# Kernel tuning notes

Measured on AMD Instinct MI355X. Metric: run time of the kernel, lower is better.

Reference implementation:

```python
import math
import jax, jax.numpy as jnp
import numpy as np

B, L, S, H, E, D = 2, 2048, 2048, 16, 64, 64

def setup_inputs() -> dict:
    key = jax.random.key(0)
    k1, k2, k3, k4, k5 = jax.random.split(key, 5)
    return {
        "queries": jax.random.normal(k1, (B, L, H, E), dtype=jnp.float32),
        "keys": jax.random.normal(k2, (B, S, H, E), dtype=jnp.float32),
        "values": jax.random.normal(k3, (B, S, H, D), dtype=jnp.float32),
        "tau": jax.random.uniform(k4, (B, 1), dtype=jnp.float32),
        "delta": jax.random.normal(k5, (B, S), dtype=jnp.float32),
        "attn_mask": jnp.zeros((1,), dtype=jnp.bool_),
    }

def reference(queries, keys, values, tau, delta, attn_mask):
    # queries: [B,L,H,E], keys: [B,S,H,E], values: [B,S,H,D]
    # tau: [B,1] -> [B,1,1,1]; delta: [B,S] -> [B,1,1,S]
    # mask_flag=False, so attn_mask is unused. Dropout is identity at eval.
    E_ = queries.shape[-1]
    scale = 1.0 / math.sqrt(E_)
    scores = jnp.einsum('blhe,bshe->bhls', queries, keys)  # [B,H,L,S]
    scores = scores * tau[:, None, None, :]                # de-stationary scale
    scores = scores + delta[:, None, None, :]              # de-stationary shift
    A = jax.nn.softmax(scale * scores, axis=-1)            # [B,H,L,S]
    V = jnp.einsum('bhls,bshd->blhd', A, values)           # [B,L,H,D]
    return V
```

## Files before the change

kernel.cpp:

```cpp
#include <hip/hip_runtime.h>


#define Bb 2
#define Ll 2048
#define Ss 2048
#define Hh 16
#define Ee 64
#define Dd 64
#define KV 64

typedef _Float16 f16x8 __attribute__((ext_vector_type(8)));
typedef _Float16 f16x4 __attribute__((ext_vector_type(4)));
typedef __fp16 fp16x2 __attribute__((ext_vector_type(2)));
typedef float f32x4 __attribute__((ext_vector_type(4)));

union Pk2 { fp16x2 h; unsigned u; };
union PackU { unsigned u[4]; f16x8 v; };

#define GLDS(gp, lp) __builtin_amdgcn_global_load_lds( \
    (const __attribute__((address_space(1))) void*)(gp), \
    (__attribute__((address_space(3))) void*)(lp), 16, 0, 0)

__global__ __launch_bounds__(256)
void prepass_k(const float* __restrict__ K, _Float16* __restrict__ K16,
               const float* __restrict__ delta, float* __restrict__ delta2)
{
    const unsigned v = blockIdx.x * 256 + threadIdx.x;
    const unsigned e4 = v & 15;
    const unsigned h  = (v >> 4) & 15;
    const unsigned s  = (v >> 8) & (Ss - 1);
    const unsigned b  = v >> 19;
    const f32x4 src = ((const f32x4*)K)[v];
    f16x4 t;
    t[0] = (_Float16)src[0]; t[1] = (_Float16)src[1];
    t[2] = (_Float16)src[2]; t[3] = (_Float16)src[3];
    ((f16x4*)K16)[(((size_t)(b * Hh + h) * Ss + s) * 16) + e4] = t;
    if (v < (Bb * Ss) / 4) {
        f32x4 dd = ((const f32x4*)delta)[v];
        ((f32x4*)delta2)[v] = (f32x4){0.125f * dd[0], 0.125f * dd[1],
                                      0.125f * dd[2], 0.125f * dd[3]};
    }
}

__global__ __launch_bounds__(256)
void prepass_v(const float* __restrict__ V, _Float16* __restrict__ VT16)
{
    __shared__ _Float16 TL[64][66];
    const int tid  = threadIdx.x;
    const int wave = tid >> 6;
    const int lane = tid & 63;
    const int bh = blockIdx.y;
    const int b  = bh >> 4;
    const int h  = bh & 15;
    const int s0 = blockIdx.x * 64;

    #pragma unroll
    for (int rr = 0; rr < 16; ++rr) {
        const int row = wave * 16 + rr;
        TL[row][lane] = (_Float16)V[((size_t)(b * Ss + s0 + row) * Hh + h) * Dd + lane];
    }
    __syncthreads();
    const int d  = tid >> 2;
    const int sq = (tid & 3) * 16;
    union { _Float16 h[16]; f16x8 v[2]; } tmp;
    #pragma unroll
    for (int i = 0; i < 16; ++i) tmp.h[i] = TL[sq + i][d];
    f16x8* dp = (f16x8*)(VT16 + ((size_t)(b * Hh + h) * Dd + d) * Ss + s0 + sq);
    dp[0] = tmp.v[0];
    dp[1] = tmp.v[1];
}

__global__ __launch_bounds__(256)
void dsattn_fwd_v3(const float* __restrict__ Q, const _Float16* __restrict__ K16,
                   const _Float16* __restrict__ VT16, const float* __restrict__ tau,
                   const float* __restrict__ delta2, float* __restrict__ out)
{
    extern __shared__ __align__(16) unsigned char smem[];

    const int tid  = threadIdx.x;
    const int wave = tid >> 6;
    const int lane = tid & 63;
    const int lq   = lane & 15;
    const int g    = lane >> 4;

    const int bh = blockIdx.y;
    const int b  = bh >> 4;
    const int h  = bh & 15;
    const int q0 = blockIdx.x * 64;

    const float alpha = 0.125f * tau[b];

    f16x8 aq[2];
    {
        const float* qp = Q + (((size_t)b * Ll + q0 + wave * 16 + lq) * Hh + h) * Ee;
        #pragma unroll
        for (int es = 0; es < 2; ++es) {
            const float* p = qp + es * 32 + g * 8;
            f16x8 t;
            #pragma unroll
            for (int j = 0; j < 8; ++j) t[j] = (_Float16)p[j];
            aq[es] = t;
        }
    }

    f32x4 osum[4];
    #pragma unroll
    for (int i = 0; i < 4; ++i) osum[i] = (f32x4){0.f, 0.f, 0.f, 0.f};
    float m_run = -1e30f, l_run = 0.0f;

    const unsigned char* kb  = (const unsigned char*)(K16 + (size_t)(b * Hh + h) * Ss * Ee);
    const unsigned char* vtb = (const unsigned char*)(VT16 + (size_t)(b * Hh + h) * Dd * Ss);
    const float* d2b = delta2 + (size_t)b * Ss;

    const int row0  = tid >> 3;
    const int slotS = (tid & 7) ^ (row0 & 7);

    {
        unsigned char* kw = smem + wave * 1024;
        unsigned char* vw = smem + 8192 + wave * 1024;
        GLDS(kb + (size_t)row0 * 128 + slotS * 16,        kw);
        GLDS(kb + (size_t)(row0 + 32) * 128 + slotS * 16, kw + 4096);
        GLDS(vtb + (size_t)row0 * (Ss * 2) + slotS * 16,        vw);
        GLDS(vtb + (size_t)(row0 + 32) * (Ss * 2) + slotS * 16, vw + 4096);
    }
    f32x4 dcur[4], dnxt[4];
    #pragma unroll
    for (int t = 0; t < 4; ++t)
        dcur[t] = *(const f32x4*)(d2b + t * 16 + 4 * g);
    __syncthreads();

    int cur = 0;
    for (int sb = 0; sb < Ss; sb += KV) {
        const int nb = (sb + KV < Ss);
        if (nb) {
            unsigned char* kw = smem + (cur ^ 1) * 16384 + wave * 1024;
            unsigned char* vw = kw + 8192;
            const int sn = sb + KV;
            GLDS(kb + (size_t)(sn + row0) * 128 + slotS * 16,        kw);
            GLDS(kb + (size_t)(sn + row0 + 32) * 128 + slotS * 16,   kw + 4096);
            GLDS(vtb + (size_t)row0 * (Ss * 2) + sn * 2 + slotS * 16,        vw);
            GLDS(vtb + (size_t)(row0 + 32) * (Ss * 2) + sn * 2 + slotS * 16, vw + 4096);
        }
        {
            const int sn = nb ? sb + KV : sb;
            #pragma unroll
            for (int t = 0; t < 4; ++t)
                dnxt[t] = *(const f32x4*)(d2b + sn + t * 16 + 4 * g);
        }

        const unsigned char* Ksm = smem + cur * 16384;
        const unsigned char* Vsm = Ksm + 8192;

        float p[16];
        float tmax = -1e30f;
        __builtin_amdgcn_s_setprio(1);
        f32x4 c4[4];
        #pragma unroll
        for (int t = 0; t < 4; ++t) {
            f32x4 c = (f32x4){0.f, 0.f, 0.f, 0.f};
            const int srow = t * 16 + lq;
            #pragma unroll
            for (int es = 0; es < 2; ++es) {
                const int slot = (es * 4 + g) ^ (srow & 7);
                f16x8 ak = *(const f16x8*)(Ksm + srow * 128 + slot * 16);
                c = __builtin_amdgcn_mfma_f32_16x16x32_f16(ak, aq[es], c, 0, 0, 0);
            }
            c4[t] = c;
        }
        __builtin_amdgcn_s_setprio(0);
        #pragma unroll
        for (int t = 0; t < 4; ++t)
            #pragma unroll
            for (int j = 0; j < 4; ++j) {
                float z = fmaf(alpha, c4[t][j], dcur[t][j]);
                p[t * 4 + j] = z;
                tmax = fmaxf(tmax, z);
            }

        tmax = fmaxf(tmax, __shfl_xor(tmax, 16));
        tmax = fmaxf(tmax, __shfl_xor(tmax, 32));
        if (!__all(tmax <= m_run + 8.0f)) {
            const float m_new = fmaxf(m_run, tmax);
            const float corr  = __expf(m_run - m_new);
            l_run *= corr;
            #pragma unroll
            for (int dt = 0; dt < 4; ++dt)
                #pragma unroll
                for (int j = 0; j < 4; ++j)
                    osum[dt][j] *= corr;
            m_run = m_new;
        }
        float psum = 0.f;
        #pragma unroll
        for (int i = 0; i < 16; ++i) { p[i] = __expf(p[i] - m_run); psum += p[i]; }
        psum += __shfl_xor(psum, 16);
        psum += __shfl_xor(psum, 32);
        l_run += psum;

        unsigned pk[8];
        #pragma unroll
        for (int t = 0; t < 4; ++t) {
            Pk2 u0, u1;
            u0.h = __builtin_amdgcn_cvt_pkrtz(p[4 * t], p[4 * t + 1]);
            u1.h = __builtin_amdgcn_cvt_pkrtz(p[4 * t + 2], p[4 * t + 3]);
            pk[t * 2] = u0.u;
            pk[t * 2 + 1] = u1.u;
        }
        const int srcA = lq + 32 * (g & 1);
        const int srcB = srcA + 16;
        const bool gh = (g >> 1);
        PackU bp[2];
        #pragma unroll
        for (int ks = 0; ks < 2; ++ks) {
            unsigned a0 = __shfl(pk[ks * 4 + 0], srcA), a1 = __shfl(pk[ks * 4 + 1], srcA);
            unsigned a2 = __shfl(pk[ks * 4 + 2], srcA), a3 = __shfl(pk[ks * 4 + 3], srcA);
            unsigned b0 = __shfl(pk[ks * 4 + 0], srcB), b1 = __shfl(pk[ks * 4 + 1], srcB);
            unsigned b2 = __shfl(pk[ks * 4 + 2], srcB), b3 = __shfl(pk[ks * 4 + 3], srcB);
            bp[ks].u[0] = gh ? a2 : a0;
            bp[ks].u[1] = gh ? a3 : a1;
            bp[ks].u[2] = gh ? b2 : b0;
            bp[ks].u[3] = gh ? b3 : b1;
        }

        __builtin_amdgcn_s_setprio(1);
        #pragma unroll
        for (int ks = 0; ks < 2; ++ks)
            #pragma unroll
            for (int dt = 0; dt < 4; ++dt) {
                const int vrow = dt * 16 + lq;
                const int slot = (ks * 4 + g) ^ (vrow & 7);
                f16x8 av = *(const f16x8*)(Vsm + vrow * 128 + slot * 16);
                osum[dt] = __builtin_amdgcn_mfma_f32_16x16x32_f16(av, bp[ks].v, osum[dt], 0, 0, 0);
            }
        __builtin_amdgcn_s_setprio(0);

        __syncthreads();
        cur ^= 1;
        #pragma unroll
        for (int t = 0; t < 4; ++t) dcur[t] = dnxt[t];
    }

    float (*Osm)[16][68] = (float (*)[16][68])smem;
    const float inv = 1.0f / l_run;
    #pragma unroll
    for (int dt = 0; dt < 4; ++dt)
        #pragma unroll
        for (int j = 0; j < 4; ++j)
            Osm[wave][lq][dt * 16 + 4 * g + j] = osum[dt][j] * inv;
    __syncthreads();
    {
        float* ob = out + (((size_t)b * Ll + q0 + wave * 16) * Hh + h) * Dd;
        #pragma unroll
        for (int r = 0; r < 16; ++r)
            ob[(size_t)r * (Hh * Dd) + lane] = Osm[wave][r][lane];
    }
}

__global__ __launch_bounds__(256)
void dsattn_fwd(const float* __restrict__ Q, const float* __restrict__ K,
                const float* __restrict__ V, const float* __restrict__ tau,
                const float* __restrict__ delta, float* __restrict__ out)
{
    __shared__ __align__(16) unsigned char Ksm[32 * 128];
    __shared__ __align__(16) unsigned char VTsm[64 * 80];
    __shared__ float dsm[32];
    __shared__ float Osm[4][16][68];

    const int tid  = threadIdx.x;
    const int wave = tid >> 6;
    const int lane = tid & 63;
    const int lq   = lane & 15;
    const int g    = lane >> 4;

    const int bh = blockIdx.y;
    const int b  = bh >> 4;
    const int h  = bh & 15;
    const int q0 = blockIdx.x * 64;

    const float alpha = 0.125f * tau[b];

    f16x8 aq[2];
    {
        const float* qp = Q + (((long)b * Ll + q0 + wave * 16 + lq) * Hh + h) * Ee;
        #pragma unroll
        for (int es = 0; es < 2; ++es) {
            const float* p = qp + es * 32 + g * 8;
            f16x8 t;
            #pragma unroll
            for (int j = 0; j < 8; ++j) t[j] = (_Float16)p[j];
            aq[es] = t;
        }
    }

    f32x4 osum[4];
    #pragma unroll
    for (int i = 0; i < 4; ++i) osum[i] = (f32x4){0.f, 0.f, 0.f, 0.f};
    float m_run = -1e30f, l_run = 0.0f;

    const float* kb = K + ((long)b * Ss * Hh + h) * Ee;
    const float* vb = V + ((long)b * Ss * Hh + h) * Dd;
    const float* db = delta + (long)b * Ss;

    const int kr    = tid >> 3;
    const int kc    = (tid & 7) * 8;
    const int kslot = (((tid & 7) ^ (kr & 7)) * 16);
    const int vd    = tid & 63;
    const int vsh   = tid >> 6;

    for (int sb = 0; sb < Ss; sb += 32) {
        __syncthreads();
        {
            const float* src = kb + (long)(sb + kr) * (Hh * Ee) + kc;
            f16x8 t;
            #pragma unroll
            for (int j = 0; j < 8; ++j) t[j] = (_Float16)src[j];
            *(f16x8*)(Ksm + kr * 128 + kslot) = t;
        }
        {
            const float* src = vb + (long)(sb + vsh * 8) * (Hh * Dd) + vd;
            f16x8 t;
            #pragma unroll
            for (int j = 0; j < 8; ++j) t[j] = (_Float16)src[j * (Hh * Dd)];
            *(f16x8*)(VTsm + vd * 80 + vsh * 16) = t;
        }
        if (tid < 32) dsm[tid] = 0.125f * db[sb + tid];
        __syncthreads();

        float p[8];
        float tmax = -1e30f;
        #pragma unroll
        for (int t = 0; t < 2; ++t) {
            f32x4 c = (f32x4){0.f, 0.f, 0.f, 0.f};
            #pragma unroll
            for (int es = 0; es < 2; ++es) {
                const int srow = t * 16 + lq;
                const int slot = ((es * 4 + g) ^ (srow & 7)) * 16;
                f16x8 ak = *(const f16x8*)(Ksm + srow * 128 + slot);
                c = __builtin_amdgcn_mfma_f32_16x16x32_f16(ak, aq[es], c, 0, 0, 0);
            }
            #pragma unroll
            for (int j = 0; j < 4; ++j) {
                float z = alpha * c[j] + dsm[t * 16 + 4 * g + j];
                p[t * 4 + j] = z;
                tmax = fmaxf(tmax, z);
            }
        }
        tmax = fmaxf(tmax, __shfl_xor(tmax, 16));
        tmax = fmaxf(tmax, __shfl_xor(tmax, 32));
        const float m_new = fmaxf(m_run, tmax);
        const float corr  = __expf(m_run - m_new);
        float psum = 0.f;
        #pragma unroll
        for (int i = 0; i < 8; ++i) { p[i] = __expf(p[i] - m_new); psum += p[i]; }
        psum += __shfl_xor(psum, 16);
        psum += __shfl_xor(psum, 32);
        l_run = l_run * corr + psum;
        m_run = m_new;
        #pragma unroll
        for (int dt = 0; dt < 4; ++dt)
            #pragma unroll
            for (int j = 0; j < 4; ++j)
                osum[dt][j] *= corr;

        Pk2 u00, u01, u10, u11;
        u00.h = __builtin_amdgcn_cvt_pkrtz(p[0], p[1]);
        u01.h = __builtin_amdgcn_cvt_pkrtz(p[2], p[3]);
        u10.h = __builtin_amdgcn_cvt_pkrtz(p[4], p[5]);
        u11.h = __builtin_amdgcn_cvt_pkrtz(p[6], p[7]);
        const int srcA = lq + 32 * (g & 1);
        const int srcB = srcA + 16;
        unsigned a00 = __shfl(u00.u, srcA), a01 = __shfl(u01.u, srcA);
        unsigned a10 = __shfl(u10.u, srcA), a11 = __shfl(u11.u, srcA);
        unsigned b00 = __shfl(u00.u, srcB), b01 = __shfl(u01.u, srcB);
        unsigned b10 = __shfl(u10.u, srcB), b11 = __shfl(u11.u, srcB);
        const bool hi = (g >= 2);
        PackU bp;
        bp.u[0] = hi ? a10 : a00;
        bp.u[1] = hi ? a11 : a01;
        bp.u[2] = hi ? b10 : b00;
        bp.u[3] = hi ? b11 : b01;

        #pragma unroll
        for (int dt = 0; dt < 4; ++dt) {
            f16x8 av = *(const f16x8*)(VTsm + (dt * 16 + lq) * 80 + g * 16);
            osum[dt] = __builtin_amdgcn_mfma_f32_16x16x32_f16(av, bp.v, osum[dt], 0, 0, 0);
        }
    }

    const float inv = 1.0f / l_run;
    #pragma unroll
    for (int dt = 0; dt < 4; ++dt)
        #pragma unroll
        for (int j = 0; j < 4; ++j)
            Osm[wave][lq][dt * 16 + 4 * g + j] = osum[dt][j] * inv;
    __syncthreads();
    {
        float* ob = out + (((long)b * Ll + q0 + wave * 16) * Hh + h) * Dd;
        #pragma unroll
        for (int r = 0; r < 16; ++r)
            ob[(long)r * (Hh * Dd) + lane] = Osm[wave][r][lane];
    }
}

extern "C" void kernel_launch(void* const* d_in, const int* in_sizes, int n_in,
                              void* d_out, int out_size, void* d_ws, size_t ws_size,
                              hipStream_t stream) {
    const float* Q     = (const float*)d_in[0];
    const float* K     = (const float*)d_in[1];
    const float* V     = (const float*)d_in[2];
    const float* tau   = (const float*)d_in[3];
    const float* delta = (const float*)d_in[4];
    float* out = (float*)d_out;

    const size_t elems = (size_t)Bb * Hh * Ss * Ee;
    const size_t need  = elems * 2 * 2 + (size_t)Bb * Ss * 4;
    dim3 grid(Ll / 64, Bb * Hh);

    if (ws_size >= need) {
        _Float16* K16    = (_Float16*)d_ws;
        _Float16* VT16   = K16 + elems;
        float*    delta2 = (float*)(VT16 + elems);
        hipLaunchKernelGGL(prepass_k, dim3(elems / 4 / 256), dim3(256), 0, stream,
                           K, K16, delta, delta2);
        hipLaunchKernelGGL(prepass_v, dim3(Ss / 64, Bb * Hh), dim3(256), 0, stream, V, VT16);
        hipLaunchKernelGGL(dsattn_fwd_v3, grid, dim3(256), 32768, stream,
                           Q, K16, VT16, tau, delta2, out);
    } else {
        hipLaunchKernelGGL(dsattn_fwd, grid, dim3(256), 0, stream, Q, K, V, tau, delta, out);
    }
}
```

Baseline: 95.96 us.

## Process two query groups per wave to reuse K/V tiles across MFMAs

Each wave now handles 32 query rows as two 16-row groups, so the block tile grows to 128 queries. Every K and V fragment loaded from LDS now feeds two MFMAs, and each query row gets its own online-softmax state. This aims to halve the K/V global and LDS traffic per query and to give the scheduler more independent MFMA work. The trade-off is higher register pressure and half as many blocks in the grid.

```diff
diff --git a/kernel.cpp b/kernel.cpp
--- a/kernel.cpp
+++ b/kernel.cpp
@@ -71,7 +71,7 @@
 }
 
 __global__ __launch_bounds__(256)
-void dsattn_fwd_v3(const float* __restrict__ Q, const _Float16* __restrict__ K16,
+void dsattn_fwd_v4(const float* __restrict__ Q, const _Float16* __restrict__ K16,
                    const _Float16* __restrict__ VT16, const float* __restrict__ tau,
                    const float* __restrict__ delta2, float* __restrict__ out)
 {
@@ -86,27 +86,32 @@
     const int bh = blockIdx.y;
     const int b  = bh >> 4;
     const int h  = bh & 15;
-    const int q0 = blockIdx.x * 64;
+    const int q0 = blockIdx.x * 128;
+    const int qw = q0 + wave * 32;
 
     const float alpha = 0.125f * tau[b];
 
-    f16x8 aq[2];
-    {
-        const float* qp = Q + (((size_t)b * Ll + q0 + wave * 16 + lq) * Hh + h) * Ee;
+    f16x8 aq[2][2];
+    #pragma unroll
+    for (int qg = 0; qg < 2; ++qg) {
+        const float* qp = Q + (((size_t)b * Ll + qw + qg * 16 + lq) * Hh + h) * Ee;
         #pragma unroll
         for (int es = 0; es < 2; ++es) {
             const float* p = qp + es * 32 + g * 8;
             f16x8 t;
             #pragma unroll
             for (int j = 0; j < 8; ++j) t[j] = (_Float16)p[j];
-            aq[es] = t;
-        }
-    }
-
-    f32x4 osum[4];
-    #pragma unroll
-    for (int i = 0; i < 4; ++i) osum[i] = (f32x4){0.f, 0.f, 0.f, 0.f};
-    float m_run = -1e30f, l_run = 0.0f;
+            aq[qg][es] = t;
+        }
+    }
+
+    f32x4 osum[2][4];
+    #pragma unroll
+    for (int qg = 0; qg < 2; ++qg)
+        #pragma unroll
+        for (int i = 0; i < 4; ++i) osum[qg][i] = (f32x4){0.f, 0.f, 0.f, 0.f};
+    float m_run[2] = {-1e30f, -1e30f};
+    float l_run[2] = {0.0f, 0.0f};
 
     const unsigned char* kb  = (const unsigned char*)(K16 + (size_t)(b * Hh + h) * Ss * Ee);
     const unsigned char* vtb = (const unsigned char*)(VT16 + (size_t)(b * Hh + h) * Dd * Ss);
@@ -128,6 +133,10 @@
     for (int t = 0; t < 4; ++t)
         dcur[t] = *(const f32x4*)(d2b + t * 16 + 4 * g);
     __syncthreads();
+
+    const int srcA = lq + 32 * (g & 1);
+    const int srcB = srcA + 16;
+    const bool gh = (g >> 1);
 
     int cur = 0;
     for (int sb = 0; sb < Ss; sb += KV) {
@@ -151,75 +160,78 @@
         const unsigned char* Ksm = smem + cur * 16384;
         const unsigned char* Vsm = Ksm + 8192;
 
-        float p[16];
-        float tmax = -1e30f;
+        f32x4 c4[2][4];
+        #pragma unroll
+        for (int qg = 0; qg < 2; ++qg)
+            #pragma unroll
+            for (int t = 0; t < 4; ++t) c4[qg][t] = (f32x4){0.f, 0.f, 0.f, 0.f};
         __builtin_amdgcn_s_setprio(1);
-        f32x4 c4[4];
         #pragma unroll
         for (int t = 0; t < 4; ++t) {
-            f32x4 c = (f32x4){0.f, 0.f, 0.f, 0.f};
             const int srow = t * 16 + lq;
             #pragma unroll
             for (int es = 0; es < 2; ++es) {
                 const int slot = (es * 4 + g) ^ (srow & 7);
                 f16x8 ak = *(const f16x8*)(Ksm + srow * 128 + slot * 16);
-                c = __builtin_amdgcn_mfma_f32_16x16x32_f16(ak, aq[es], c, 0, 0, 0);
-            }
-            c4[t] = c;
+                c4[0][t] = __builtin_amdgcn_mfma_f32_16x16x32_f16(ak, aq[0][es], c4[0][t], 0, 0, 0);
+                c4[1][t] = __builtin_amdgcn_mfma_f32_16x16x32_f16(ak, aq[1][es], c4[1][t], 0, 0, 0);
+            }
         }
         __builtin_amdgcn_s_setprio(0);
-        #pragma unroll
-        for (int t = 0; t < 4; ++t)
-            #pragma unroll
-            for (int j = 0; j < 4; ++j) {
-                float z = fmaf(alpha, c4[t][j], dcur[t][j]);
-                p[t * 4 + j] = z;
-                tmax = fmaxf(tmax, z);
-            }
-
-        tmax = fmaxf(tmax, __shfl_xor(tmax, 16));
-        tmax = fmaxf(tmax, __shfl_xor(tmax, 32));
-        if (!__all(tmax <= m_run + 8.0f)) {
-            const float m_new = fmaxf(m_run, tmax);
-            const float corr  = __expf(m_run - m_new);
-            l_run *= corr;
-            #pragma unroll
-            for (int dt = 0; dt < 4; ++dt)
+
+        PackU bp[2][2];
+        #pragma unroll
+        for (int qg = 0; qg < 2; ++qg) {
+            float p[16];
+            float tmax = -1e30f;
+            #pragma unroll
+            for (int t = 0; t < 4; ++t)
                 #pragma unroll
-                for (int j = 0; j < 4; ++j)
-                    osum[dt][j] *= corr;
-            m_run = m_new;
-        }
-        float psum = 0.f;
-        #pragma unroll
-        for (int i = 0; i < 16; ++i) { p[i] = __expf(p[i] - m_run); psum += p[i]; }
-        psum += __shfl_xor(psum, 16);
-        psum += __shfl_xor(psum, 32);
-        l_run += psum;
-
-        unsigned pk[8];
-        #pragma unroll
-        for (int t = 0; t < 4; ++t) {
-            Pk2 u0, u1;
-            u0.h = __builtin_amdgcn_cvt_pkrtz(p[4 * t], p[4 * t + 1]);
-            u1.h = __builtin_amdgcn_cvt_pkrtz(p[4 * t + 2], p[4 * t + 3]);
-            pk[t * 2] = u0.u;
-            pk[t * 2 + 1] = u1.u;
-        }
-        const int srcA = lq + 32 * (g & 1);
-        const int srcB = srcA + 16;
-        const bool gh = (g >> 1);
-        PackU bp[2];
-        #pragma unroll
-        for (int ks = 0; ks < 2; ++ks) {
-            unsigned a0 = __shfl(pk[ks * 4 + 0], srcA), a1 = __shfl(pk[ks * 4 + 1], srcA);
-            unsigned a2 = __shfl(pk[ks * 4 + 2], srcA), a3 = __shfl(pk[ks * 4 + 3], srcA);
-            unsigned b0 = __shfl(pk[ks * 4 + 0], srcB), b1 = __shfl(pk[ks * 4 + 1], srcB);
-            unsigned b2 = __shfl(pk[ks * 4 + 2], srcB), b3 = __shfl(pk[ks * 4 + 3], srcB);
-            bp[ks].u[0] = gh ? a2 : a0;
-            bp[ks].u[1] = gh ? a3 : a1;
-            bp[ks].u[2] = gh ? b2 : b0;
-            bp[ks].u[3] = gh ? b3 : b1;
+                for (int j = 0; j < 4; ++j) {
+                    float z = fmaf(alpha, c4[qg][t][j], dcur[t][j]);
+                    p[t * 4 + j] = z;
+                    tmax = fmaxf(tmax, z);
+                }
+            tmax = fmaxf(tmax, __shfl_xor(tmax, 16));
+            tmax = fmaxf(tmax, __shfl_xor(tmax, 32));
+            if (!__all(tmax <= m_run[qg] + 8.0f)) {
+                const float m_new = fmaxf(m_run[qg], tmax);
+                const float corr  = __expf(m_run[qg] - m_new);
+                l_run[qg] *= corr;
+                #pragma unroll
+                for (int dt = 0; dt < 4; ++dt)
+                    #pragma unroll
+                    for (int j = 0; j < 4; ++j)
+                        osum[qg][dt][j] *= corr;
+                m_run[qg] = m_new;
+            }
+            float psum = 0.f;
+            #pragma unroll
+            for (int i = 0; i < 16; ++i) { p[i] = __expf(p[i] - m_run[qg]); psum += p[i]; }
+            psum += __shfl_xor(psum, 16);
+            psum += __shfl_xor(psum, 32);
+            l_run[qg] += psum;
+
+            unsigned pk[8];
+            #pragma unroll
+            for (int t = 0; t < 4; ++t) {
+                Pk2 u0, u1;
+                u0.h = __builtin_amdgcn_cvt_pkrtz(p[4 * t], p[4 * t + 1]);
+                u1.h = __builtin_amdgcn_cvt_pkrtz(p[4 * t + 2], p[4 * t + 3]);
+                pk[t * 2] = u0.u;
+                pk[t * 2 + 1] = u1.u;
+            }
+            #pragma unroll
+            for (int ks = 0; ks < 2; ++ks) {
+                unsigned a0 = __shfl(pk[ks * 4 + 0], srcA), a1 = __shfl(pk[ks * 4 + 1], srcA);
+                unsigned a2 = __shfl(pk[ks * 4 + 2], srcA), a3 = __shfl(pk[ks * 4 + 3], srcA);
+                unsigned b0 = __shfl(pk[ks * 4 + 0], srcB), b1 = __shfl(pk[ks * 4 + 1], srcB);
+                unsigned b2 = __shfl(pk[ks * 4 + 2], srcB), b3 = __shfl(pk[ks * 4 + 3], srcB);
+                bp[qg][ks].u[0] = gh ? a2 : a0;
+                bp[qg][ks].u[1] = gh ? a3 : a1;
+                bp[qg][ks].u[2] = gh ? b2 : b0;
+                bp[qg][ks].u[3] = gh ? b3 : b1;
+            }
         }
 
         __builtin_amdgcn_s_setprio(1);
@@ -230,7 +242,8 @@
                 const int vrow = dt * 16 + lq;
                 const int slot = (ks * 4 + g) ^ (vrow & 7);
                 f16x8 av = *(const f16x8*)(Vsm + vrow * 128 + slot * 16);
-                osum[dt] = __builtin_amdgcn_mfma_f32_16x16x32_f16(av, bp[ks].v, osum[dt], 0, 0, 0);
+                osum[0][dt] = __builtin_amdgcn_mfma_f32_16x16x32_f16(av, bp[0][ks].v, osum[0][dt], 0, 0, 0);
+                osum[1][dt] = __builtin_amdgcn_mfma_f32_16x16x32_f16(av, bp[1][ks].v, osum[1][dt], 0, 0, 0);
             }
         __builtin_amdgcn_s_setprio(0);
 
@@ -240,18 +253,21 @@
         for (int t = 0; t < 4; ++t) dcur[t] = dnxt[t];
     }
 
-    float (*Osm)[16][68] = (float (*)[16][68])smem;
-    const float inv = 1.0f / l_run;
-    #pragma unroll
-    for (int dt = 0; dt < 4; ++dt)
-        #pragma unroll
-        for (int j = 0; j < 4; ++j)
-            Osm[wave][lq][dt * 16 + 4 * g + j] = osum[dt][j] * inv;
+    float (*Osm)[32][68] = (float (*)[32][68])smem;
+    #pragma unroll
+    for (int qg = 0; qg < 2; ++qg) {
+        const float inv = 1.0f / l_run[qg];
+        #pragma unroll
+        for (int dt = 0; dt < 4; ++dt)
+            #pragma unroll
+            for (int j = 0; j < 4; ++j)
+                Osm[wave][qg * 16 + lq][dt * 16 + 4 * g + j] = osum[qg][dt][j] * inv;
+    }
     __syncthreads();
     {
-        float* ob = out + (((size_t)b * Ll + q0 + wave * 16) * Hh + h) * Dd;
-        #pragma unroll
-        for (int r = 0; r < 16; ++r)
+        float* ob = out + (((size_t)b * Ll + qw) * Hh + h) * Dd;
+        #pragma unroll
+        for (int r = 0; r < 32; ++r)
             ob[(size_t)r * (Hh * Dd) + lane] = Osm[wave][r][lane];
     }
 }
@@ -414,7 +430,6 @@
 
     const size_t elems = (size_t)Bb * Hh * Ss * Ee;
     const size_t need  = elems * 2 * 2 + (size_t)Bb * Ss * 4;
-    dim3 grid(Ll / 64, Bb * Hh);
 
     if (ws_size >= need) {
         _Float16* K16    = (_Float16*)d_ws;
@@ -423,9 +438,10 @@
         hipLaunchKernelGGL(prepass_k, dim3(elems / 4 / 256), dim3(256), 0, stream,
                            K, K16, delta, delta2);
         hipLaunchKernelGGL(prepass_v, dim3(Ss / 64, Bb * Hh), dim3(256), 0, stream, V, VT16);
-        hipLaunchKernelGGL(dsattn_fwd_v3, grid, dim3(256), 32768, stream,
+        hipLaunchKernelGGL(dsattn_fwd_v4, dim3(Ll / 128, Bb * Hh), dim3(256), 34816, stream,
                            Q, K16, VT16, tau, delta2, out);
     } else {
-        hipLaunchKernelGGL(dsattn_fwd, grid, dim3(256), 0, stream, Q, K, V, tau, delta, out);
+        hipLaunchKernelGGL(dsattn_fwd, dim3(Ll / 64, Bb * Hh), dim3(256), 0, stream,
+                           Q, K, V, tau, delta, out);
     }
 }
```

New measurement: 95.27 us. About the same (-0.7%).
